# Kernel tuning notes

Hardware: AMD Instinct MI355X
Metric: run time of the kernel (lower is better)

Reference implementation:

```python
import jax, jax.numpy as jnp
import numpy as np

N = 30000      # nodes
E = 480000     # edges (before self-loops)
D = 100        # hidden_dim / in_channels
H = 4          # heads
PH = 100       # per-head dim
L = 6          # layers
G = 128        # graphs in batch
NUM_ATOM = 100
OUT_DIM = 64


def _xavier(k, shape, gain=1.0):
    fan_in, fan_out = shape[-1], shape[-2]
    lim = gain * np.sqrt(6.0 / (fan_in + fan_out))
    return jax.random.uniform(k, shape, jnp.float32, -lim, lim)


def setup_inputs() -> dict:
    key = jax.random.key(0)
    ks = jax.random.split(key, 12)
    x = jax.random.randint(ks[0], (N,), 0, NUM_ATOM)
    edge_index = jax.random.randint(ks[1], (2, E), 0, N)
    edge_attr = jax.random.normal(ks[2], (E, D), dtype=jnp.float32)
    batch = jnp.sort(jax.random.randint(ks[3], (N,), 0, G))
    emb = _xavier(ks[4], (NUM_ATOM, D))
    W = _xavier(ks[5], (L, H * PH, D))
    We = _xavier(ks[6], (L, H * PH, D))
    a = _xavier(ks[7], (L, H, 2 * PH), gain=1.414)
    ln_g = jnp.ones((L, D), jnp.float32)
    ln_b = jnp.zeros((L, D), jnp.float32)
    w1 = _xavier(ks[8], (OUT_DIM, D))
    b1 = jnp.zeros((OUT_DIM,), jnp.float32)
    w2 = _xavier(ks[9], (1, OUT_DIM))
    b2 = jnp.zeros((1,), jnp.float32)
    return dict(x=x, edge_index=edge_index, edge_attr=edge_attr, batch=batch,
                emb=emb, W=W, We=We, a=a, ln_g=ln_g, ln_b=ln_b,
                w1=w1, b1=b1, w2=w2, b2=b2)


def _forward(x, edge_index, edge_attr, batch, emb, W, We, a, ln_g, ln_b, w1, b1, w2, b2):
    n = x.shape[0]
    loop = jnp.arange(n)
    src = jnp.concatenate([edge_index[0], loop])            # [E']
    dst = jnp.concatenate([edge_index[1], loop])            # [E']  (target, softmax key)
    ea = jnp.concatenate([edge_attr, jnp.zeros((n, D), edge_attr.dtype)], axis=0)  # self-loop attr = 0
    h = emb[x]                                              # [N, D]
    for l in range(L):
        hx = (h @ W[l].T).reshape(n, H, PH)                 # [N, H, PH]
        he = (ea @ We[l].T).reshape(-1, H, PH)              # [E', H, PH]
        a_i, a_j = a[l][:, :PH], a[l][:, PH:]               # [H, PH] each
        # alpha = sum(a * [x_i ; x_j + edge_attr]) split into two dots
        score_i = jnp.einsum('nhd,hd->nh', hx, a_i)         # [N, H]
        xj = hx[src]                                        # [E', H, PH]
        alpha = score_i[dst] + jnp.einsum('ehd,hd->eh', xj + he, a_j)  # [E', H]
        alpha = jnp.where(alpha > 0, alpha, 0.2 * alpha)    # leaky_relu(0.2)
        # segment softmax over edges grouped by target node (every node has a self-loop)
        amax = jax.ops.segment_max(alpha, dst, num_segments=n)
        alpha = jnp.exp(alpha - amax[dst])
        denom = jax.ops.segment_sum(alpha, dst, num_segments=n)
        alpha = alpha / (denom[dst] + 1e-16)
        msg = (xj * alpha[..., None]).sum(axis=1)           # [E', PH] (heads summed, per module)
        aggr = jax.ops.segment_sum(msg, dst, num_segments=n)  # [N, PH]
        # LayerNorm(D), eps=1e-5
        mu = aggr.mean(-1, keepdims=True)
        var = ((aggr - mu) ** 2).mean(-1, keepdims=True)
        y = (aggr - mu) / jnp.sqrt(var + 1e-5) * ln_g[l] + ln_b[l]
        y = jax.nn.elu(y)                                   # dropout = identity (eval)
        h = y + h
    # global mean pool over graphs
    s = jax.ops.segment_sum(h, batch, num_segments=G)
    cnt = jax.ops.segment_sum(jnp.ones((n, 1), h.dtype), batch, num_segments=G)
    pooled = s / jnp.maximum(cnt, 1.0)
    hh = pooled @ w1.T + b1                                 # [G, 64]
    out = hh @ w2.T + b2                                    # [G, 1]
    return out, hh


def reference(x, edge_index, edge_attr, batch, emb, W, We, a, ln_g, ln_b, w1, b1, w2, b2):
    return _forward(x, edge_index, edge_attr, batch, emb, W, We, a, ln_g, ln_b, w1, b1, w2, b2)
```

## Files before the change

kernel.cpp:

```cpp
#include <hip/hip_runtime.h>
#include <cstdint>
#include <cstddef>

#define N_NODES 30000
#define N_EDGES 480000
#define EP_EDGES (N_EDGES + N_NODES)
#define DIM 100
#define NH 4
#define NL 6
#define NG 128
#define KP 416

#define OFF_H       0u
#define OFF_AGG2    12000000u
#define OFF_EID     12000000u
#define OFF_DEG     14040000u
#define OFF_CURS    14160000u
#define OFF_ETMP    16000000u
#define OFF_POOL    12000000u
#define OFF_CNT     12051200u
#define OFF_SCI     60000000u
#define OFF_SCJ     60480000u
#define OFF_ESC     60960000u
#define OFF_CWIJ    85440000u
#define OFF_WR      85469184u
#define OFF_INDPTR  86429184u
#define OFF_CSRS    86549248u
#define OFF_BSUM    88589248u
#define OFF_BW      88589376u

typedef _Float16 half8 __attribute__((ext_vector_type(8)));
typedef __fp16 fp16x2 __attribute__((ext_vector_type(2)));
typedef float f32x4 __attribute__((ext_vector_type(4)));

static __device__ __forceinline__ unsigned short f2h(float f) {
  return __builtin_bit_cast(unsigned short, (_Float16)f);
}
static __device__ __forceinline__ float h2f(unsigned short u) {
  return (float)__builtin_bit_cast(_Float16, u);
}

__global__ __launch_bounds__(256) void k_init(const int* __restrict__ x,
                                              const float* __restrict__ emb,
                                              float* __restrict__ h,
                                              int* __restrict__ deg, int* __restrict__ cursor) {
  int tid = blockIdx.x * 256 + threadIdx.x;
  if (tid < N_NODES * DIM) {
    int n = tid / DIM;
    int d = tid - n * DIM;
    h[tid] = emb[x[n] * DIM + d];
  }
  if (tid < N_NODES) { deg[tid] = 0; cursor[tid] = 0; }
}

__global__ __launch_bounds__(256) void k_fold(const float* __restrict__ W,
                                              const float* __restrict__ We,
                                              const float* __restrict__ a,
                                              float* __restrict__ cWij,
                                              unsigned short* __restrict__ Bw) {
  int tid = blockIdx.x * 256 + threadIdx.x;
  if (tid < NL * DIM * 8) {
    int l = tid / 800, r = tid % 800;
    int k = r >> 3, c = r & 7;
    int hh = c & 3, isJ = c >> 2;
    const float* wp = W + (size_t)(l * 400 + hh * 100) * 100 + k;
    const float* ap = a + (size_t)(l * 4 + hh) * 200 + isJ * 100;
    float s = 0.f;
    for (int d = 0; d < 100; ++d) s += wp[(size_t)d * 100] * ap[d];
    cWij[l * 800 + k * 8 + c] = s;
  } else if (tid < NL * DIM * 8 + DIM * 24) {
    int m = tid - NL * DIM * 8;
    int k = m / 24, c = m % 24;
    int l = c >> 2, hh = c & 3;
    const float* wp = We + (size_t)(l * 400 + hh * 100) * 100 + k;
    const float* ap = a + (size_t)(l * 4 + hh) * 200 + 100;
    float s = 0.f;
    for (int d = 0; d < 100; ++d) s += wp[(size_t)d * 100] * ap[d];
    _Float16 vh = (_Float16)s;
    _Float16 vl = (_Float16)(s - (float)vh);
    int ct = c >> 4;
    int lane = (((k & 31) >> 3) << 4) | (c & 15);
    int ks = k >> 5;
    int j = k & 7;
    Bw[(size_t)(((0 * 2 + ct) * 4 + ks) * 64 + lane) * 8 + j] = __builtin_bit_cast(unsigned short, vh);
    Bw[(size_t)(((1 * 2 + ct) * 4 + ks) * 64 + lane) * 8 + j] = __builtin_bit_cast(unsigned short, vl);
  } else if (tid < NL * DIM * 8 + DIM * 24 + 8192) {
    int E = tid - (NL * DIM * 8 + DIM * 24);
    int j = E & 7;
    int lane = (E >> 3) & 63;
    int rest = E >> 9;
    int ks = rest & 3;
    int ct = (rest >> 2) & 1;
    int c = ct * 16 + (lane & 15);
    int k = ks * 32 + ((lane >> 4) << 3) + j;
    if (!(c < 24 && k < 100)) Bw[E] = 0;
  }
}

__global__ __launch_bounds__(256) void k_bfrag(const float* __restrict__ W,
                                               unsigned short* __restrict__ Bfrag) {
  int tid = blockIdx.x * 256 + threadIdx.x;
  if (tid >= NL * 7 * 13 * 64 * 8) return;
  int j = tid & 7;
  int lane = (tid >> 3) & 63;
  int rest = tid >> 9;
  int ks = rest % 13;
  int rest2 = rest / 13;
  int ct = rest2 % 7;
  int l = rest2 / 7;
  int k = ks * 32 + ((lane >> 4) << 3) + j;
  int n = ct * 16 + (lane & 15);
  float v = 0.f;
  if (k < 400 && n < 100) {
    int hh = k / 100, kk = k - hh * 100;
    v = W[(size_t)(l * 400 + hh * 100 + n) * 100 + kk];
  }
  Bfrag[tid] = f2h(v);
}

__global__ __launch_bounds__(256) void k_deg(const int* __restrict__ ei, int* __restrict__ deg) {
  int tid = blockIdx.x * 256 + threadIdx.x;
  if (tid >= EP_EDGES) return;
  int dstn = (tid < N_EDGES) ? ei[N_EDGES + tid] : (tid - N_EDGES);
  atomicAdd(&deg[dstn], 1);
}

__global__ __launch_bounds__(1024) void k_scan1(const int* __restrict__ deg,
                                                int* __restrict__ indptr, int* __restrict__ bsum) {
  __shared__ int s[1024];
  int t = threadIdx.x;
  int i = blockIdx.x * 1024 + t;
  int v = (i < N_NODES) ? deg[i] : 0;
  s[t] = v;
  __syncthreads();
  for (int off = 1; off < 1024; off <<= 1) {
    int tmp = (t >= off) ? s[t - off] : 0;
    __syncthreads();
    s[t] += tmp;
    __syncthreads();
  }
  if (i < N_NODES) indptr[i + 1] = s[t];
  if (t == 1023) bsum[blockIdx.x] = s[1023];
}
__global__ __launch_bounds__(64) void k_scan2(int* __restrict__ bsum) {
  int t = threadIdx.x;
  int v = (t < 30) ? bsum[t] : 0;
  int inc = v;
  for (int off = 1; off < 64; off <<= 1) {
    int up = __shfl_up(inc, off);
    if (t >= off) inc += up;
  }
  if (t < 30) bsum[t] = inc - v;
}
__global__ __launch_bounds__(1024) void k_scan3(int* __restrict__ indptr,
                                                const int* __restrict__ bsum) {
  int i = blockIdx.x * 1024 + threadIdx.x;
  if (i < N_NODES) indptr[i + 1] += bsum[blockIdx.x];
  if (i == 0) indptr[0] = 0;
}

__global__ __launch_bounds__(256) void k_scatter(const int* __restrict__ ei,
                                                 const int* __restrict__ indptr,
                                                 int* __restrict__ cursor,
                                                 int* __restrict__ csr_src,
                                                 int* __restrict__ csr_eid) {
  int tid = blockIdx.x * 256 + threadIdx.x;
  if (tid >= EP_EDGES) return;
  int dstn = (tid < N_EDGES) ? ei[N_EDGES + tid] : (tid - N_EDGES);
  int srcn = (tid < N_EDGES) ? ei[tid] : (tid - N_EDGES);
  int p = indptr[dstn] + atomicAdd(&cursor[dstn], 1);
  csr_src[p] = srcn;
  csr_eid[p] = (tid < N_EDGES) ? tid : -1;
}

__global__ __launch_bounds__(256, 4) void k_escore(const float* __restrict__ ea,
                                                   const unsigned short* __restrict__ Bw,
                                                   unsigned short* __restrict__ esc_tmp) {
  __shared__ __align__(16) float s_ea[64 * 128];
  int t = threadIdx.x;
  int lane = t & 63;
  int wv = t >> 6;

  const half8* bp = (const half8*)Bw;
  half8 Bh[2][4], Bl[2][4];
#pragma unroll
  for (int ct = 0; ct < 2; ++ct)
#pragma unroll
    for (int ks = 0; ks < 4; ++ks) {
      Bh[ct][ks] = bp[((0 * 2 + ct) * 4 + ks) * 64 + lane];
      Bl[ct][ks] = bp[((1 * 2 + ct) * 4 + ks) * 64 + lane];
    }

  int e0 = blockIdx.x * 64;
  const float4* g4 = (const float4*)(ea + (size_t)e0 * 100);
  for (int z = t; z < 448; z += 256) {
    int zr = z / 7, zc = z - zr * 7;
    int o = 400 + zc * 16;
    *(float4*)((char*)s_ea + zr * 512 + (o ^ ((zr & 7) << 4))) = (float4){0.f, 0.f, 0.f, 0.f};
  }
#pragma unroll
  for (int i = 0; i < 7; ++i) {
    int v = i * 256 + t;
    if (i < 6 || v < 1600) {
      float4 val = g4[v];
      int r = v / 25, kk = v - r * 25;
      *(float4*)((char*)s_ea + r * 512 + ((kk * 16) ^ ((r & 7) << 4))) = val;
    }
  }
  __syncthreads();

  int c = lane & 15;
  int quad = lane >> 4;
  int lrow = wv * 16 + c;
  int swz = (lrow & 7) << 4;
  const char* base = (const char*)s_ea + lrow * 512;
  f32x4 acc0 = (f32x4){0.f, 0.f, 0.f, 0.f};
  f32x4 acc1 = (f32x4){0.f, 0.f, 0.f, 0.f};
#pragma unroll
  for (int ks = 0; ks < 4; ++ks) {
    int o = ks * 128 + quad * 32;
    float4 xa = *(const float4*)(base + ((o) ^ swz));
    float4 xb = *(const float4*)(base + ((o + 16) ^ swz));
    fp16x2 h0 = __builtin_amdgcn_cvt_pkrtz(xa.x, xa.y);
    fp16x2 h1 = __builtin_amdgcn_cvt_pkrtz(xa.z, xa.w);
    fp16x2 h2 = __builtin_amdgcn_cvt_pkrtz(xb.x, xb.y);
    fp16x2 h3 = __builtin_amdgcn_cvt_pkrtz(xb.z, xb.w);
    fp16x2 l0 = __builtin_amdgcn_cvt_pkrtz(xa.x - (float)h0[0], xa.y - (float)h0[1]);
    fp16x2 l1 = __builtin_amdgcn_cvt_pkrtz(xa.z - (float)h1[0], xa.w - (float)h1[1]);
    fp16x2 l2 = __builtin_amdgcn_cvt_pkrtz(xb.x - (float)h2[0], xb.y - (float)h2[1]);
    fp16x2 l3 = __builtin_amdgcn_cvt_pkrtz(xb.z - (float)h3[0], xb.w - (float)h3[1]);
    uint4 uh = {__builtin_bit_cast(unsigned, h0), __builtin_bit_cast(unsigned, h1),
                __builtin_bit_cast(unsigned, h2), __builtin_bit_cast(unsigned, h3)};
    uint4 ul = {__builtin_bit_cast(unsigned, l0), __builtin_bit_cast(unsigned, l1),
                __builtin_bit_cast(unsigned, l2), __builtin_bit_cast(unsigned, l3)};
    half8 xh = __builtin_bit_cast(half8, uh);
    half8 xl = __builtin_bit_cast(half8, ul);
    acc0 = __builtin_amdgcn_mfma_f32_16x16x32_f16(xh, Bh[0][ks], acc0, 0, 0, 0);
    acc0 = __builtin_amdgcn_mfma_f32_16x16x32_f16(xl, Bh[0][ks], acc0, 0, 0, 0);
    acc0 = __builtin_amdgcn_mfma_f32_16x16x32_f16(xh, Bl[0][ks], acc0, 0, 0, 0);
    acc1 = __builtin_amdgcn_mfma_f32_16x16x32_f16(xh, Bh[1][ks], acc1, 0, 0, 0);
    acc1 = __builtin_amdgcn_mfma_f32_16x16x32_f16(xl, Bh[1][ks], acc1, 0, 0, 0);
    acc1 = __builtin_amdgcn_mfma_f32_16x16x32_f16(xh, Bl[1][ks], acc1, 0, 0, 0);
  }

  unsigned short* orow = esc_tmp + (size_t)(e0 + wv * 16 + quad * 4) * 24;
#pragma unroll
  for (int r = 0; r < 4; ++r) {
    unsigned short* op = orow + r * 24;
    op[c] = f2h(acc0[r]);
    if (c < 8) op[16 + c] = f2h(acc1[r]);
  }
}

__global__ __launch_bounds__(256) void k_permute(const unsigned short* __restrict__ esc_tmp,
                                                 const int* __restrict__ csr_eid,
                                                 unsigned short* __restrict__ esc) {
  int p = blockIdx.x * 256 + threadIdx.x;
  if (p >= EP_EDGES) return;
  int e = csr_eid[p];
  ushort4 v[NL];
  if (e >= 0) {
    const unsigned short* rp = esc_tmp + (size_t)e * 24;
#pragma unroll
    for (int l = 0; l < NL; ++l) v[l] = *(const ushort4*)(rp + l * 4);
  } else {
#pragma unroll
    for (int l = 0; l < NL; ++l) { v[l].x = 0; v[l].y = 0; v[l].z = 0; v[l].w = 0; }
  }
#pragma unroll
  for (int l = 0; l < NL; ++l)
    *(ushort4*)(esc + ((size_t)l * EP_EDGES + p) * 4) = v[l];
}

__global__ __launch_bounds__(256) void k_score(const float* __restrict__ h,
                                               const float* __restrict__ cw,
                                               float* __restrict__ sc_i, float* __restrict__ sc_j) {
  __shared__ __align__(16) float s[DIM * 8];
  for (int i = threadIdx.x; i < DIM * 8; i += 256) s[i] = cw[i];
  __syncthreads();
  int n = blockIdx.x * 256 + threadIdx.x;
  if (n >= N_NODES) return;
  float acc[8] = {0.f, 0.f, 0.f, 0.f, 0.f, 0.f, 0.f, 0.f};
  const float* hr = h + (size_t)n * DIM;
  for (int k4 = 0; k4 < 25; ++k4) {
    float4 v = *(const float4*)(hr + k4 * 4);
    float vv[4] = {v.x, v.y, v.z, v.w};
#pragma unroll
    for (int kk = 0; kk < 4; ++kk) {
      const float* sr = s + (k4 * 4 + kk) * 8;
#pragma unroll
      for (int c = 0; c < 8; ++c) acc[c] += vv[kk] * sr[c];
    }
  }
  *(float4*)(sc_i + (size_t)n * 4) = make_float4(acc[0], acc[1], acc[2], acc[3]);
  *(float4*)(sc_j + (size_t)n * 4) = make_float4(acc[4], acc[5], acc[6], acc[7]);
}

#define ALPHA_P(pp)                                                                  \
  int s_ = csr_src[pp];                                                              \
  float4 sj_ = *(const float4*)(sc_j + (size_t)s_ * 4);                              \
  ushort4 eb_ = *(const ushort4*)(esc_l + (size_t)(pp) * 4);                         \
  float a0 = si.x + sj_.x + h2f(eb_.x); a0 = a0 > 0.f ? a0 : 0.2f * a0;              \
  float a1 = si.y + sj_.y + h2f(eb_.y); a1 = a1 > 0.f ? a1 : 0.2f * a1;              \
  float a2 = si.z + sj_.z + h2f(eb_.z); a2 = a2 > 0.f ? a2 : 0.2f * a2;              \
  float a3 = si.w + sj_.w + h2f(eb_.w); a3 = a3 > 0.f ? a3 : 0.2f * a3;

__global__ __launch_bounds__(256) void k_aggr(const float* __restrict__ h,
                                              const float* __restrict__ sc_i,
                                              const float* __restrict__ sc_j,
                                              const unsigned short* __restrict__ esc_l,
                                              const int* __restrict__ indptr,
                                              const int* __restrict__ csr_src,
                                              unsigned short* __restrict__ agg2h) {
  __shared__ __align__(16) uint4 s_pack[4][64];
  int wave = threadIdx.x >> 6;
  int lane = threadIdx.x & 63;
  int n = blockIdx.x * 4 + wave;
  int start = indptr[n], end = indptr[n + 1];
  int deg = end - start;
  float4 si = *(const float4*)(sc_i + (size_t)n * 4);
  float A0 = 0.f, A1 = 0.f, A2 = 0.f, A3 = 0.f;
  float B0 = 0.f, B1 = 0.f, B2 = 0.f, B3 = 0.f;
  bool has2 = lane < (DIM - 64);

  if (deg <= 64) {
    int p = start + lane;
    bool act = p < end;
    int srcr = 0;
    float a0 = -1e30f, a1 = -1e30f, a2 = -1e30f, a3 = -1e30f;
    if (act) {
      int s2 = csr_src[p];
      float4 sj2 = *(const float4*)(sc_j + (size_t)s2 * 4);
      ushort4 eb2 = *(const ushort4*)(esc_l + (size_t)p * 4);
      a0 = si.x + sj2.x + h2f(eb2.x); a0 = a0 > 0.f ? a0 : 0.2f * a0;
      a1 = si.y + sj2.y + h2f(eb2.y); a1 = a1 > 0.f ? a1 : 0.2f * a1;
      a2 = si.z + sj2.z + h2f(eb2.z); a2 = a2 > 0.f ? a2 : 0.2f * a2;
      a3 = si.w + sj2.w + h2f(eb2.w); a3 = a3 > 0.f ? a3 : 0.2f * a3;
      srcr = s2;
    }
    float m0 = a0, m1 = a1, m2 = a2, m3 = a3;
    for (int off = 32; off; off >>= 1) {
      m0 = fmaxf(m0, __shfl_xor(m0, off));
      m1 = fmaxf(m1, __shfl_xor(m1, off));
      m2 = fmaxf(m2, __shfl_xor(m2, off));
      m3 = fmaxf(m3, __shfl_xor(m3, off));
    }
    float e0 = act ? __expf(a0 - m0) : 0.f;
    float e1 = act ? __expf(a1 - m1) : 0.f;
    float e2 = act ? __expf(a2 - m2) : 0.f;
    float e3 = act ? __expf(a3 - m3) : 0.f;
    float d0 = e0, d1 = e1, d2 = e2, d3 = e3;
    for (int off = 32; off; off >>= 1) {
      d0 += __shfl_xor(d0, off); d1 += __shfl_xor(d1, off);
      d2 += __shfl_xor(d2, off); d3 += __shfl_xor(d3, off);
    }
    float w0 = e0 * (1.f / (d0 + 1e-16f));
    float w1 = e1 * (1.f / (d1 + 1e-16f));
    float w2 = e2 * (1.f / (d2 + 1e-16f));
    float w3 = e3 * (1.f / (d3 + 1e-16f));
    uint4 pk;
    pk.x = (unsigned)srcr;
    pk.y = (unsigned)f2h(w0) | ((unsigned)f2h(w1) << 16);
    pk.z = (unsigned)f2h(w2) | ((unsigned)f2h(w3) << 16);
    pk.w = 0u;
    s_pack[wave][lane] = pk;
    for (int j = 0; j < deg; ++j) {
      uint4 pk2 = s_pack[wave][j];
      int sj2 = (int)pk2.x;
      float q0 = h2f((unsigned short)(pk2.y & 0xffffu));
      float q1 = h2f((unsigned short)(pk2.y >> 16));
      float q2 = h2f((unsigned short)(pk2.z & 0xffffu));
      float q3 = h2f((unsigned short)(pk2.z >> 16));
      const float* hr = h + (size_t)sj2 * DIM;
      float hv0 = hr[lane];
      float hv1 = has2 ? hr[64 + lane] : 0.f;
      A0 += q0 * hv0; A1 += q1 * hv0; A2 += q2 * hv0; A3 += q3 * hv0;
      B0 += q0 * hv1; B1 += q1 * hv1; B2 += q2 * hv1; B3 += q3 * hv1;
    }
  } else {
    float m0 = -1e30f, m1 = -1e30f, m2 = -1e30f, m3 = -1e30f;
    for (int p = start + lane; p < end; p += 64) {
      ALPHA_P(p)
      (void)s_;
      m0 = fmaxf(m0, a0); m1 = fmaxf(m1, a1); m2 = fmaxf(m2, a2); m3 = fmaxf(m3, a3);
    }
    for (int off = 32; off; off >>= 1) {
      m0 = fmaxf(m0, __shfl_xor(m0, off));
      m1 = fmaxf(m1, __shfl_xor(m1, off));
      m2 = fmaxf(m2, __shfl_xor(m2, off));
      m3 = fmaxf(m3, __shfl_xor(m3, off));
    }
    float d0 = 0.f, d1 = 0.f, d2 = 0.f, d3 = 0.f;
    for (int p = start + lane; p < end; p += 64) {
      ALPHA_P(p)
      (void)s_;
      d0 += __expf(a0 - m0); d1 += __expf(a1 - m1);
      d2 += __expf(a2 - m2); d3 += __expf(a3 - m3);
    }
    for (int off = 32; off; off >>= 1) {
      d0 += __shfl_xor(d0, off); d1 += __shfl_xor(d1, off);
      d2 += __shfl_xor(d2, off); d3 += __shfl_xor(d3, off);
    }
    float i0 = 1.f / (d0 + 1e-16f), i1 = 1.f / (d1 + 1e-16f);
    float i2 = 1.f / (d2 + 1e-16f), i3 = 1.f / (d3 + 1e-16f);
    for (int base = start; base < end; base += 64) {
      int cntv = min(64, end - base);
      int p = base + lane;
      float w0 = 0.f, w1 = 0.f, w2 = 0.f, w3 = 0.f;
      int srcr = 0;
      if (p < end) {
        ALPHA_P(p)
        w0 = __expf(a0 - m0) * i0; w1 = __expf(a1 - m1) * i1;
        w2 = __expf(a2 - m2) * i2; w3 = __expf(a3 - m3) * i3;
        srcr = s_;
      }
      for (int j = 0; j < cntv; ++j) {
        int sj2 = __shfl(srcr, j);
        float q0 = __shfl(w0, j), q1 = __shfl(w1, j);
        float q2 = __shfl(w2, j), q3 = __shfl(w3, j);
        const float* hr = h + (size_t)sj2 * DIM;
        float hv0 = hr[lane];
        float hv1 = has2 ? hr[64 + lane] : 0.f;
        A0 += q0 * hv0; A1 += q1 * hv0; A2 += q2 * hv0; A3 += q3 * hv0;
        B0 += q0 * hv1; B1 += q1 * hv1; B2 += q2 * hv1; B3 += q3 * hv1;
      }
    }
  }
  unsigned short* outp = agg2h + (size_t)n * KP;
  outp[lane] = f2h(A0); outp[100 + lane] = f2h(A1);
  outp[200 + lane] = f2h(A2); outp[300 + lane] = f2h(A3);
  if (has2) {
    outp[64 + lane] = f2h(B0); outp[164 + lane] = f2h(B1);
    outp[264 + lane] = f2h(B2); outp[364 + lane] = f2h(B3);
  }
  if (lane < KP - 400) outp[400 + lane] = 0;
}

__global__ __launch_bounds__(256) void k_gemm2(const _Float16* __restrict__ agg2h,
                                               const _Float16* __restrict__ Bfrag_l,
                                               const float* __restrict__ lg,
                                               const float* __restrict__ lb,
                                               float* __restrict__ h) {
  int t = threadIdx.x;
  int lane = t & 63;
  int w = t >> 6;
  int c = lane & 15;
  int quad = lane >> 4;
  int nb = blockIdx.x * 64 + w * 16;

  f32x4 acc[7];
#pragma unroll
  for (int ct = 0; ct < 7; ++ct) acc[ct] = (f32x4){0.f, 0.f, 0.f, 0.f};

  const _Float16* arow = agg2h + (size_t)(nb + c) * KP + quad * 8;
#pragma unroll
  for (int ks = 0; ks < 13; ++ks) {
    half8 a = *(const half8*)(arow + ks * 32);
    const _Float16* bp = Bfrag_l + (size_t)(ks * 64 + lane) * 8;
#pragma unroll
    for (int ct = 0; ct < 7; ++ct) {
      half8 b = *(const half8*)(bp + (size_t)ct * 13 * 64 * 8);
      acc[ct] = __builtin_amdgcn_mfma_f32_16x16x32_f16(a, b, acc[ct], 0, 0, 0);
    }
  }

  float gv[7], bv[7];
#pragma unroll
  for (int ct = 0; ct < 7; ++ct) {
    int col = ct * 16 + c;
    gv[ct] = (col < DIM) ? lg[col] : 0.f;
    bv[ct] = (col < DIM) ? lb[col] : 0.f;
  }
  bool c4 = c < 4;
#pragma unroll
  for (int r = 0; r < 4; ++r) {
    int n = nb + quad * 4 + r;
    float v[7];
#pragma unroll
    for (int ct = 0; ct < 7; ++ct) v[ct] = acc[ct][r];
    float s = v[0] + v[1] + v[2] + v[3] + v[4] + v[5] + (c4 ? v[6] : 0.f);
    s += __shfl_xor(s, 1); s += __shfl_xor(s, 2);
    s += __shfl_xor(s, 4); s += __shfl_xor(s, 8);
    float mu = s * 0.01f;
    float dv[7];
    float s2 = 0.f;
#pragma unroll
    for (int ct = 0; ct < 6; ++ct) { dv[ct] = v[ct] - mu; s2 += dv[ct] * dv[ct]; }
    dv[6] = c4 ? (v[6] - mu) : 0.f;
    s2 += dv[6] * dv[6];
    s2 += __shfl_xor(s2, 1); s2 += __shfl_xor(s2, 2);
    s2 += __shfl_xor(s2, 4); s2 += __shfl_xor(s2, 8);
    float rstd = rsqrtf(s2 * 0.01f + 1e-5f);
    if (n < N_NODES) {
      float* hp = h + (size_t)n * DIM;
#pragma unroll
      for (int ct = 0; ct < 7; ++ct) {
        int col = ct * 16 + c;
        if (ct < 6 || c4) {
          float y = dv[ct] * rstd * gv[ct] + bv[ct];
          y = y > 0.f ? y : (__expf(y) - 1.f);
          hp[col] += y;
        }
      }
    }
  }
}

__global__ __launch_bounds__(128) void k_pool(const float* __restrict__ h,
                                              const int* __restrict__ batch,
                                              float* __restrict__ pooled, float* __restrict__ cnt) {
  int d = threadIdx.x;
  int n0 = blockIdx.x * 64;
  int n1 = min(n0 + 64, N_NODES);
  if (n0 >= N_NODES) return;
  int curg = -1;
  float acc = 0.f, c = 0.f;
  for (int n = n0; n < n1; ++n) {
    int g = batch[n];
    if (g != curg) {
      if (curg >= 0) {
        if (d < 100) atomicAdd(&pooled[(size_t)curg * DIM + d], acc);
        if (d == 0) atomicAdd(&cnt[curg], c);
      }
      curg = g; acc = 0.f; c = 0.f;
    }
    if (d < 100) acc += h[(size_t)n * DIM + d];
    c += 1.f;
  }
  if (curg >= 0) {
    if (d < 100) atomicAdd(&pooled[(size_t)curg * DIM + d], acc);
    if (d == 0) atomicAdd(&cnt[curg], c);
  }
}

__global__ __launch_bounds__(64) void k_mlp(const float* __restrict__ pooled,
                                            const float* __restrict__ cnt,
                                            const float* __restrict__ w1, const float* __restrict__ b1,
                                            const float* __restrict__ w2, const float* __restrict__ b2,
                                            float* __restrict__ out) {
  int g = blockIdx.x;
  int j = threadIdx.x;
  float invc = 1.0f / fmaxf(cnt[g], 1.0f);
  const float* pr = pooled + (size_t)g * DIM;
  const float* wr = w1 + (size_t)j * DIM;
  float acc = 0.f;
  for (int k = 0; k < DIM; ++k) acc += pr[k] * wr[k];
  float hh = acc * invc + b1[j];
  out[NG + g * 64 + j] = hh;
  float v = hh * w2[j];
  for (int off = 32; off; off >>= 1) v += __shfl_xor(v, off);
  if (j == 0) out[g] = v + b2[0];
}

extern "C" void kernel_launch(void* const* d_in, const int* in_sizes, int n_in,
                              void* d_out, int out_size, void* d_ws, size_t ws_size,
                              hipStream_t stream) {
  (void)in_sizes; (void)n_in; (void)out_size; (void)ws_size;
  const int* x = (const int*)d_in[0];
  const int* ei = (const int*)d_in[1];
  const float* ea = (const float*)d_in[2];
  const int* batch = (const int*)d_in[3];
  const float* emb = (const float*)d_in[4];
  const float* W = (const float*)d_in[5];
  const float* We = (const float*)d_in[6];
  const float* a = (const float*)d_in[7];
  const float* ln_g = (const float*)d_in[8];
  const float* ln_b = (const float*)d_in[9];
  const float* w1 = (const float*)d_in[10];
  const float* b1 = (const float*)d_in[11];
  const float* w2 = (const float*)d_in[12];
  const float* b2 = (const float*)d_in[13];
  float* outp = (float*)d_out;

  char* ws = (char*)d_ws;
  float* h = (float*)(ws + OFF_H);
  unsigned short* agg2h = (unsigned short*)(ws + OFF_AGG2);
  int* csr_eid = (int*)(ws + OFF_EID);
  int* deg = (int*)(ws + OFF_DEG);
  int* cursor = (int*)(ws + OFF_CURS);
  unsigned short* esc_tmp = (unsigned short*)(ws + OFF_ETMP);
  float* pooled = (float*)(ws + OFF_POOL);
  float* cnt = (float*)(ws + OFF_CNT);
  float* sc_i = (float*)(ws + OFF_SCI);
  float* sc_j = (float*)(ws + OFF_SCJ);
  unsigned short* esc = (unsigned short*)(ws + OFF_ESC);
  float* cWij = (float*)(ws + OFF_CWIJ);
  unsigned short* Bw = (unsigned short*)(ws + OFF_BW);
  unsigned short* Bfrag = (unsigned short*)(ws + OFF_WR);
  int* indptr = (int*)(ws + OFF_INDPTR);
  int* csr_src = (int*)(ws + OFF_CSRS);
  int* bsum = (int*)(ws + OFF_BSUM);

  k_init<<<11719, 256, 0, stream>>>(x, emb, h, deg, cursor);
  k_fold<<<61, 256, 0, stream>>>(W, We, a, cWij, Bw);
  k_bfrag<<<1092, 256, 0, stream>>>(W, Bfrag);
  k_deg<<<1993, 256, 0, stream>>>(ei, deg);
  k_scan1<<<30, 1024, 0, stream>>>(deg, indptr, bsum);
  k_scan2<<<1, 64, 0, stream>>>(bsum);
  k_scan3<<<30, 1024, 0, stream>>>(indptr, bsum);
  k_scatter<<<1993, 256, 0, stream>>>(ei, indptr, cursor, csr_src, csr_eid);
  k_escore<<<7500, 256, 0, stream>>>(ea, Bw, esc_tmp);
  k_permute<<<1993, 256, 0, stream>>>(esc_tmp, csr_eid, esc);

  for (int l = 0; l < NL; ++l) {
    k_score<<<118, 256, 0, stream>>>(h, cWij + l * 800, sc_i, sc_j);
    k_aggr<<<7500, 256, 0, stream>>>(h, sc_i, sc_j, esc + (size_t)l * EP_EDGES * 4,
                                     indptr, csr_src, agg2h);
    k_gemm2<<<469, 256, 0, stream>>>((const _Float16*)agg2h,
                                     (const _Float16*)(Bfrag + (size_t)l * 7 * 13 * 64 * 8),
                                     ln_g + l * 100, ln_b + l * 100, h);
  }

  hipMemsetAsync(ws + OFF_POOL, 0, 51200 + 512, stream);
  k_pool<<<469, 128, 0, stream>>>(h, batch, pooled, cnt);
  k_mlp<<<128, 64, 0, stream>>>(pooled, cnt, w1, b1, w2, b2, outp);
}
```

Measured before the change: 829.0 us.

## Process four nodes per wave in aggregation with interleaved gather loops

Each wave of the aggregation kernel now handles four destination nodes instead of one. It computes softmax weights for all four into shared memory, then runs a single gather loop that interleaves the neighbour-row loads of the four nodes. The goal is more independent memory requests in flight per wave and less per-wave setup, to hide the latency of the feature gathers. In exchange it holds four sets of accumulators, which raises register pressure, launches a quarter as many blocks, and leaves lanes idle when the four nodes have uneven degrees.

```diff
diff --git a/kernel.cpp b/kernel.cpp
--- a/kernel.cpp
+++ b/kernel.cpp
@@ -312,128 +312,162 @@
                                               const int* __restrict__ indptr,
                                               const int* __restrict__ csr_src,
                                               unsigned short* __restrict__ agg2h) {
-  __shared__ __align__(16) uint4 s_pack[4][64];
+  __shared__ __align__(16) uint4 s_pack[4][4][64];
   int wave = threadIdx.x >> 6;
   int lane = threadIdx.x & 63;
-  int n = blockIdx.x * 4 + wave;
-  int start = indptr[n], end = indptr[n + 1];
-  int deg = end - start;
-  float4 si = *(const float4*)(sc_i + (size_t)n * 4);
-  float A0 = 0.f, A1 = 0.f, A2 = 0.f, A3 = 0.f;
-  float B0 = 0.f, B1 = 0.f, B2 = 0.f, B3 = 0.f;
+  int nb = (blockIdx.x * 4 + wave) * 4;
   bool has2 = lane < (DIM - 64);
 
-  if (deg <= 64) {
-    int p = start + lane;
-    bool act = p < end;
-    int srcr = 0;
-    float a0 = -1e30f, a1 = -1e30f, a2 = -1e30f, a3 = -1e30f;
-    if (act) {
-      int s2 = csr_src[p];
-      float4 sj2 = *(const float4*)(sc_j + (size_t)s2 * 4);
-      ushort4 eb2 = *(const ushort4*)(esc_l + (size_t)p * 4);
-      a0 = si.x + sj2.x + h2f(eb2.x); a0 = a0 > 0.f ? a0 : 0.2f * a0;
-      a1 = si.y + sj2.y + h2f(eb2.y); a1 = a1 > 0.f ? a1 : 0.2f * a1;
-      a2 = si.z + sj2.z + h2f(eb2.z); a2 = a2 > 0.f ? a2 : 0.2f * a2;
-      a3 = si.w + sj2.w + h2f(eb2.w); a3 = a3 > 0.f ? a3 : 0.2f * a3;
-      srcr = s2;
-    }
-    float m0 = a0, m1 = a1, m2 = a2, m3 = a3;
-    for (int off = 32; off; off >>= 1) {
-      m0 = fmaxf(m0, __shfl_xor(m0, off));
-      m1 = fmaxf(m1, __shfl_xor(m1, off));
-      m2 = fmaxf(m2, __shfl_xor(m2, off));
-      m3 = fmaxf(m3, __shfl_xor(m3, off));
-    }
-    float e0 = act ? __expf(a0 - m0) : 0.f;
-    float e1 = act ? __expf(a1 - m1) : 0.f;
-    float e2 = act ? __expf(a2 - m2) : 0.f;
-    float e3 = act ? __expf(a3 - m3) : 0.f;
-    float d0 = e0, d1 = e1, d2 = e2, d3 = e3;
-    for (int off = 32; off; off >>= 1) {
-      d0 += __shfl_xor(d0, off); d1 += __shfl_xor(d1, off);
-      d2 += __shfl_xor(d2, off); d3 += __shfl_xor(d3, off);
-    }
-    float w0 = e0 * (1.f / (d0 + 1e-16f));
-    float w1 = e1 * (1.f / (d1 + 1e-16f));
-    float w2 = e2 * (1.f / (d2 + 1e-16f));
-    float w3 = e3 * (1.f / (d3 + 1e-16f));
-    uint4 pk;
-    pk.x = (unsigned)srcr;
-    pk.y = (unsigned)f2h(w0) | ((unsigned)f2h(w1) << 16);
-    pk.z = (unsigned)f2h(w2) | ((unsigned)f2h(w3) << 16);
-    pk.w = 0u;
-    s_pack[wave][lane] = pk;
-    for (int j = 0; j < deg; ++j) {
-      uint4 pk2 = s_pack[wave][j];
-      int sj2 = (int)pk2.x;
-      float q0 = h2f((unsigned short)(pk2.y & 0xffffu));
-      float q1 = h2f((unsigned short)(pk2.y >> 16));
-      float q2 = h2f((unsigned short)(pk2.z & 0xffffu));
-      float q3 = h2f((unsigned short)(pk2.z >> 16));
-      const float* hr = h + (size_t)sj2 * DIM;
-      float hv0 = hr[lane];
-      float hv1 = has2 ? hr[64 + lane] : 0.f;
-      A0 += q0 * hv0; A1 += q1 * hv0; A2 += q2 * hv0; A3 += q3 * hv0;
-      B0 += q0 * hv1; B1 += q1 * hv1; B2 += q2 * hv1; B3 += q3 * hv1;
-    }
-  } else {
-    float m0 = -1e30f, m1 = -1e30f, m2 = -1e30f, m3 = -1e30f;
-    for (int p = start + lane; p < end; p += 64) {
-      ALPHA_P(p)
-      (void)s_;
-      m0 = fmaxf(m0, a0); m1 = fmaxf(m1, a1); m2 = fmaxf(m2, a2); m3 = fmaxf(m3, a3);
-    }
-    for (int off = 32; off; off >>= 1) {
-      m0 = fmaxf(m0, __shfl_xor(m0, off));
-      m1 = fmaxf(m1, __shfl_xor(m1, off));
-      m2 = fmaxf(m2, __shfl_xor(m2, off));
-      m3 = fmaxf(m3, __shfl_xor(m3, off));
-    }
-    float d0 = 0.f, d1 = 0.f, d2 = 0.f, d3 = 0.f;
-    for (int p = start + lane; p < end; p += 64) {
-      ALPHA_P(p)
-      (void)s_;
-      d0 += __expf(a0 - m0); d1 += __expf(a1 - m1);
-      d2 += __expf(a2 - m2); d3 += __expf(a3 - m3);
-    }
-    for (int off = 32; off; off >>= 1) {
-      d0 += __shfl_xor(d0, off); d1 += __shfl_xor(d1, off);
-      d2 += __shfl_xor(d2, off); d3 += __shfl_xor(d3, off);
-    }
-    float i0 = 1.f / (d0 + 1e-16f), i1 = 1.f / (d1 + 1e-16f);
-    float i2 = 1.f / (d2 + 1e-16f), i3 = 1.f / (d3 + 1e-16f);
-    for (int base = start; base < end; base += 64) {
-      int cntv = min(64, end - base);
-      int p = base + lane;
-      float w0 = 0.f, w1 = 0.f, w2 = 0.f, w3 = 0.f;
+  float A0[4], A1[4], A2[4], A3[4];
+  float C0[4], C1[4], C2[4], C3[4];
+  int degf[4];
+
+#pragma unroll
+  for (int r = 0; r < 4; ++r) {
+    int n = nb + r;
+    int start = indptr[n], end = indptr[n + 1];
+    int deg = end - start;
+    float4 si = *(const float4*)(sc_i + (size_t)n * 4);
+    A0[r] = A1[r] = A2[r] = A3[r] = 0.f;
+    C0[r] = C1[r] = C2[r] = C3[r] = 0.f;
+
+    if (deg <= 64) {
+      int p = start + lane;
+      bool act = p < end;
       int srcr = 0;
-      if (p < end) {
+      float a0 = -1e30f, a1 = -1e30f, a2 = -1e30f, a3 = -1e30f;
+      if (act) {
+        int s2 = csr_src[p];
+        float4 sj2 = *(const float4*)(sc_j + (size_t)s2 * 4);
+        ushort4 eb2 = *(const ushort4*)(esc_l + (size_t)p * 4);
+        a0 = si.x + sj2.x + h2f(eb2.x); a0 = a0 > 0.f ? a0 : 0.2f * a0;
+        a1 = si.y + sj2.y + h2f(eb2.y); a1 = a1 > 0.f ? a1 : 0.2f * a1;
+        a2 = si.z + sj2.z + h2f(eb2.z); a2 = a2 > 0.f ? a2 : 0.2f * a2;
+        a3 = si.w + sj2.w + h2f(eb2.w); a3 = a3 > 0.f ? a3 : 0.2f * a3;
+        srcr = s2;
+      }
+      float m0 = a0, m1 = a1, m2 = a2, m3 = a3;
+      for (int off = 32; off; off >>= 1) {
+        m0 = fmaxf(m0, __shfl_xor(m0, off));
+        m1 = fmaxf(m1, __shfl_xor(m1, off));
+        m2 = fmaxf(m2, __shfl_xor(m2, off));
+        m3 = fmaxf(m3, __shfl_xor(m3, off));
+      }
+      float e0 = act ? __expf(a0 - m0) : 0.f;
+      float e1 = act ? __expf(a1 - m1) : 0.f;
+      float e2 = act ? __expf(a2 - m2) : 0.f;
+      float e3 = act ? __expf(a3 - m3) : 0.f;
+      float d0 = e0, d1 = e1, d2 = e2, d3 = e3;
+      for (int off = 32; off; off >>= 1) {
+        d0 += __shfl_xor(d0, off); d1 += __shfl_xor(d1, off);
+        d2 += __shfl_xor(d2, off); d3 += __shfl_xor(d3, off);
+      }
+      float w0 = e0 * (1.f / (d0 + 1e-16f));
+      float w1 = e1 * (1.f / (d1 + 1e-16f));
+      float w2 = e2 * (1.f / (d2 + 1e-16f));
+      float w3 = e3 * (1.f / (d3 + 1e-16f));
+      uint4 pk;
+      pk.x = (unsigned)srcr;
+      pk.y = (unsigned)f2h(w0) | ((unsigned)f2h(w1) << 16);
+      pk.z = (unsigned)f2h(w2) | ((unsigned)f2h(w3) << 16);
+      pk.w = 0u;
+      s_pack[wave][r][lane] = pk;
+      degf[r] = deg;
+    } else {
+      degf[r] = 0;
+      float m0 = -1e30f, m1 = -1e30f, m2 = -1e30f, m3 = -1e30f;
+      for (int p = start + lane; p < end; p += 64) {
         ALPHA_P(p)
-        w0 = __expf(a0 - m0) * i0; w1 = __expf(a1 - m1) * i1;
-        w2 = __expf(a2 - m2) * i2; w3 = __expf(a3 - m3) * i3;
-        srcr = s_;
-      }
-      for (int j = 0; j < cntv; ++j) {
-        int sj2 = __shfl(srcr, j);
-        float q0 = __shfl(w0, j), q1 = __shfl(w1, j);
-        float q2 = __shfl(w2, j), q3 = __shfl(w3, j);
+        (void)s_;
+        m0 = fmaxf(m0, a0); m1 = fmaxf(m1, a1); m2 = fmaxf(m2, a2); m3 = fmaxf(m3, a3);
+      }
+      for (int off = 32; off; off >>= 1) {
+        m0 = fmaxf(m0, __shfl_xor(m0, off));
+        m1 = fmaxf(m1, __shfl_xor(m1, off));
+        m2 = fmaxf(m2, __shfl_xor(m2, off));
+        m3 = fmaxf(m3, __shfl_xor(m3, off));
+      }
+      float d0 = 0.f, d1 = 0.f, d2 = 0.f, d3 = 0.f;
+      for (int p = start + lane; p < end; p += 64) {
+        ALPHA_P(p)
+        (void)s_;
+        d0 += __expf(a0 - m0); d1 += __expf(a1 - m1);
+        d2 += __expf(a2 - m2); d3 += __expf(a3 - m3);
+      }
+      for (int off = 32; off; off >>= 1) {
+        d0 += __shfl_xor(d0, off); d1 += __shfl_xor(d1, off);
+        d2 += __shfl_xor(d2, off); d3 += __shfl_xor(d3, off);
+      }
+      float i0 = 1.f / (d0 + 1e-16f), i1 = 1.f / (d1 + 1e-16f);
+      float i2 = 1.f / (d2 + 1e-16f), i3 = 1.f / (d3 + 1e-16f);
+      float gA0 = 0.f, gA1 = 0.f, gA2 = 0.f, gA3 = 0.f;
+      float gB0 = 0.f, gB1 = 0.f, gB2 = 0.f, gB3 = 0.f;
+      for (int base = start; base < end; base += 64) {
+        int cntv = min(64, end - base);
+        int p = base + lane;
+        float w0 = 0.f, w1 = 0.f, w2 = 0.f, w3 = 0.f;
+        int srcr = 0;
+        if (p < end) {
+          ALPHA_P(p)
+          w0 = __expf(a0 - m0) * i0; w1 = __expf(a1 - m1) * i1;
+          w2 = __expf(a2 - m2) * i2; w3 = __expf(a3 - m3) * i3;
+          srcr = s_;
+        }
+        for (int j = 0; j < cntv; ++j) {
+          int sj2 = __shfl(srcr, j);
+          float q0 = __shfl(w0, j), q1 = __shfl(w1, j);
+          float q2 = __shfl(w2, j), q3 = __shfl(w3, j);
+          const float* hr = h + (size_t)sj2 * DIM;
+          float hv0 = hr[lane];
+          float hv1 = has2 ? hr[64 + lane] : 0.f;
+          gA0 += q0 * hv0; gA1 += q1 * hv0; gA2 += q2 * hv0; gA3 += q3 * hv0;
+          gB0 += q0 * hv1; gB1 += q1 * hv1; gB2 += q2 * hv1; gB3 += q3 * hv1;
+        }
+      }
+      unsigned short* outp = agg2h + (size_t)n * KP;
+      outp[lane] = f2h(gA0); outp[100 + lane] = f2h(gA1);
+      outp[200 + lane] = f2h(gA2); outp[300 + lane] = f2h(gA3);
+      if (has2) {
+        outp[64 + lane] = f2h(gB0); outp[164 + lane] = f2h(gB1);
+        outp[264 + lane] = f2h(gB2); outp[364 + lane] = f2h(gB3);
+      }
+      if (lane < KP - 400) outp[400 + lane] = 0;
+    }
+  }
+
+  int dmax = max(max(degf[0], degf[1]), max(degf[2], degf[3]));
+  for (int j = 0; j < dmax; ++j) {
+#pragma unroll
+    for (int r = 0; r < 4; ++r) {
+      if (j < degf[r]) {
+        uint4 pk2 = s_pack[wave][r][j];
+        int sj2 = (int)pk2.x;
+        float q0 = h2f((unsigned short)(pk2.y & 0xffffu));
+        float q1 = h2f((unsigned short)(pk2.y >> 16));
+        float q2 = h2f((unsigned short)(pk2.z & 0xffffu));
+        float q3 = h2f((unsigned short)(pk2.z >> 16));
         const float* hr = h + (size_t)sj2 * DIM;
         float hv0 = hr[lane];
         float hv1 = has2 ? hr[64 + lane] : 0.f;
-        A0 += q0 * hv0; A1 += q1 * hv0; A2 += q2 * hv0; A3 += q3 * hv0;
-        B0 += q0 * hv1; B1 += q1 * hv1; B2 += q2 * hv1; B3 += q3 * hv1;
-      }
-    }
-  }
-  unsigned short* outp = agg2h + (size_t)n * KP;
-  outp[lane] = f2h(A0); outp[100 + lane] = f2h(A1);
-  outp[200 + lane] = f2h(A2); outp[300 + lane] = f2h(A3);
-  if (has2) {
-    outp[64 + lane] = f2h(B0); outp[164 + lane] = f2h(B1);
-    outp[264 + lane] = f2h(B2); outp[364 + lane] = f2h(B3);
-  }
-  if (lane < KP - 400) outp[400 + lane] = 0;
+        A0[r] += q0 * hv0; A1[r] += q1 * hv0; A2[r] += q2 * hv0; A3[r] += q3 * hv0;
+        C0[r] += q0 * hv1; C1[r] += q1 * hv1; C2[r] += q2 * hv1; C3[r] += q3 * hv1;
+      }
+    }
+  }
+
+#pragma unroll
+  for (int r = 0; r < 4; ++r) {
+    if (degf[r] > 0) {
+      unsigned short* outp = agg2h + (size_t)(nb + r) * KP;
+      outp[lane] = f2h(A0[r]); outp[100 + lane] = f2h(A1[r]);
+      outp[200 + lane] = f2h(A2[r]); outp[300 + lane] = f2h(A3[r]);
+      if (has2) {
+        outp[64 + lane] = f2h(C0[r]); outp[164 + lane] = f2h(C1[r]);
+        outp[264 + lane] = f2h(C2[r]); outp[364 + lane] = f2h(C3[r]);
+      }
+      if (lane < KP - 400) outp[400 + lane] = 0;
+    }
+  }
 }
 
 __global__ __launch_bounds__(256) void k_gemm2(const _Float16* __restrict__ agg2h,
@@ -604,7 +638,7 @@
 
   for (int l = 0; l < NL; ++l) {
     k_score<<<118, 256, 0, stream>>>(h, cWij + l * 800, sc_i, sc_j);
-    k_aggr<<<7500, 256, 0, stream>>>(h, sc_i, sc_j, esc + (size_t)l * EP_EDGES * 4,
+    k_aggr<<<1875, 256, 0, stream>>>(h, sc_i, sc_j, esc + (size_t)l * EP_EDGES * 4,
                                      indptr, csr_src, agg2h);
     k_gemm2<<<469, 256, 0, stream>>>((const _Float16*)agg2h,
                                      (const _Float16*)(Bfrag + (size_t)l * 7 * 13 * 64 * 8),
```

New measurement: 953.8 us. 15.1% more time.
